# Performance work log

Measured on AMD Instinct MI355X. Metric: run time of the kernel, lower is better.

## Reference

```python
import jax, jax.numpy as jnp
import numpy as np

B, S, D = 64, 1024, 1024
NUM_TAGS = 33            # real IOBES tags
N = NUM_TAGS + 1         # + BOS tag
BOS = N - 1
NEG_INF = -10000.0


def setup_inputs() -> dict:
    key = jax.random.key(0)
    k1, k2, k3, k4 = jax.random.split(key, 4)
    emissions = jax.random.normal(k1, (B, S, D), dtype=jnp.float32)
    tags = jax.random.randint(k2, (B, S), 0, NUM_TAGS)          # valid real tags only
    mask = jnp.ones((B, S), dtype=jnp.float32)
    W = jax.random.normal(k3, (D, N), dtype=jnp.float32) / np.sqrt(D)
    b = jnp.zeros((N,), dtype=jnp.float32)
    transitions = jax.random.uniform(k4, (N, N), minval=-0.1, maxval=0.1, dtype=jnp.float32)
    # nothing may transition INTO the BOS tag
    transitions = transitions.at[:, BOS].set(NEG_INF)
    return {"emissions": emissions, "tags": tags, "mask": mask,
            "W": W, "b": b, "transitions": transitions}


def _crf_nll(em, tags, mask, transitions):
    """em: (B,S,N) projected emissions. Returns scalar NLL (sum over batch)."""
    # ---- gold path score ----
    first = tags[:, 0]                                          # (B,)
    score = transitions[BOS, first] + jnp.take_along_axis(em[:, 0], first[:, None], axis=1)[:, 0]
    e_t = jnp.take_along_axis(em[:, 1:], tags[:, 1:, None], axis=2)[..., 0]   # (B,S-1)
    t_t = transitions[tags[:, :-1], tags[:, 1:]]                 # (B,S-1)
    score = score + jnp.sum((e_t + t_t) * mask[:, 1:], axis=1)   # (B,)

    # ---- log partition via forward algorithm (scan over time) ----
    alphas0 = transitions[BOS][None, :] + em[:, 0]               # (B,N)

    def step(alphas, xs):
        em_t, m_t = xs                                           # (B,N), (B,)
        # scores[b, prev, nxt] = alphas[b,prev] + T[prev,nxt] + em_t[b,nxt]
        scores = alphas[:, :, None] + transitions[None] + em_t[:, None, :]
        new = jax.scipy.special.logsumexp(scores, axis=1)        # (B,N)
        m = m_t[:, None]
        return m * new + (1.0 - m) * alphas, None

    xs = (jnp.swapaxes(em[:, 1:], 0, 1), jnp.swapaxes(mask[:, 1:], 0, 1))  # time-major
    alphas, _ = jax.lax.scan(step, alphas0, xs)
    partition = jax.scipy.special.logsumexp(alphas, axis=1)      # (B,)
    return -jnp.sum(score - partition)


def reference(emissions, tags, mask, W, b, transitions):
    proj = emissions @ W + b                                     # (B,S,N), dropout p=0 is identity
    loss = _crf_nll(proj, tags, mask, transitions)
    logits = proj[:, :, :-1]                                     # drop BOS column, as in torch forward
    return loss, logits
```

## Files before the change

### kernel.cpp

```cpp
#include <hip/hip_runtime.h>
#include <math.h>

#define SS 1024
#define DD 1024
#define NB 64
#define NT 34
#define NP 48
#define NC 16
#define BOSR 33

typedef __attribute__((ext_vector_type(8))) short bf16x8;
typedef __attribute__((ext_vector_type(4))) float f32x4;

#define WS_BOS   0
#define WS_PMAT  (WS_BOS + NB*SS)
#define WS_CC    (WS_PMAT + NB*NC*NP*NP)
#define WS_Z     (WS_CC + NB*NC)
#define WS_SC    (WS_Z + NB)
#define WS_BF16  (WS_SC + NB)
#define BW_WT    0
#define BW_ETA   (48*1024)

__device__ __forceinline__ float warp_sum64(float x) {
  #pragma unroll
  for (int off = 32; off > 0; off >>= 1) x += __shfl_down(x, off, 64);
  return x;
}
__device__ __forceinline__ float rfl(float x) {
  return __int_as_float(__builtin_amdgcn_readfirstlane(__float_as_int(x)));
}
__device__ __forceinline__ unsigned short f2bf(float f) {
  unsigned int u = __float_as_uint(f);
  unsigned int r = u + 0x7fffu + ((u >> 16) & 1u);
  return (unsigned short)(r >> 16);
}
__device__ __forceinline__ float bf2f(unsigned short h) {
  return __uint_as_float(((unsigned int)h) << 16);
}

__global__ __launch_bounds__(256) void prep(const float* __restrict__ W,
                                            const float* __restrict__ T,
                                            unsigned short* __restrict__ bw) {
  int idx = blockIdx.x * 256 + threadIdx.x;
  if (idx < 48 * 1024) {
    int n = idx >> 10, k = idx & 1023;
    float v = (n < NT) ? W[k * NT + n] : 0.0f;
    bw[BW_WT + idx] = f2bf(v);
  } else if (idx < 48 * 1024 + 48 * 64) {
    int j = idx - 48 * 1024;
    int m = j >> 6, k = j & 63;
    float v = (m < NT && k < NT) ? __expf(T[k * NT + m]) : 0.0f;
    bw[BW_ETA + j] = f2bf(v);
  }
}

__global__ __launch_bounds__(256) void gemm_mfma(
    const float* __restrict__ em, const unsigned short* __restrict__ bw,
    const float* __restrict__ bias,
    float* __restrict__ logits, float* __restrict__ bos) {
  __shared__ unsigned short At[2][128][40];
  const int tid = threadIdx.x;
  const int lane = tid & 63, wv = tid >> 6;
  const int q = lane >> 4, l15 = lane & 15;
  const size_t row0 = (size_t)blockIdx.x * 128;
  const unsigned short* Wt = bw + BW_WT;
  const float4* g4 = (const float4*)(em + row0 * DD);

  f32x4 acc[2][3];
  f32x4 z4 = {0.f, 0.f, 0.f, 0.f};
  #pragma unroll
  for (int mt = 0; mt < 2; ++mt)
    #pragma unroll
    for (int nt = 0; nt < 3; ++nt) acc[mt][nt] = z4;

  int sr[4], sq[4];
  #pragma unroll
  for (int i = 0; i < 4; ++i) { int s = tid + i * 256; sr[i] = s >> 3; sq[i] = s & 7; }

  float4 pf[4];
  #pragma unroll
  for (int i = 0; i < 4; ++i) pf[i] = g4[sr[i] * 256 + sq[i]];
  bf16x8 Bf[3], Bn[3];
  #pragma unroll
  for (int nt = 0; nt < 3; ++nt)
    Bf[nt] = *(const bf16x8*)(Wt + (nt * 16 + l15) * 1024 + q * 8);

  for (int c = 0; c < 32; ++c) {
    #pragma unroll
    for (int i = 0; i < 4; ++i) {
      uint2 pk;
      pk.x = f2bf(pf[i].x) | ((unsigned int)f2bf(pf[i].y) << 16);
      pk.y = f2bf(pf[i].z) | ((unsigned int)f2bf(pf[i].w) << 16);
      *(uint2*)&At[c & 1][sr[i]][sq[i] * 4] = pk;
    }
    int cn = (c + 1 < 32) ? c + 1 : c;
    #pragma unroll
    for (int i = 0; i < 4; ++i) pf[i] = g4[sr[i] * 256 + cn * 8 + sq[i]];
    #pragma unroll
    for (int nt = 0; nt < 3; ++nt)
      Bn[nt] = *(const bf16x8*)(Wt + (nt * 16 + l15) * 1024 + cn * 32 + q * 8);
    __syncthreads();
    bf16x8 Af[2];
    #pragma unroll
    for (int mt = 0; mt < 2; ++mt)
      Af[mt] = *(const bf16x8*)&At[c & 1][wv * 32 + mt * 16 + l15][q * 8];
    #pragma unroll
    for (int mt = 0; mt < 2; ++mt)
      #pragma unroll
      for (int nt = 0; nt < 3; ++nt)
        acc[mt][nt] = __builtin_amdgcn_mfma_f32_16x16x32_bf16(
            Af[mt], Bf[nt], acc[mt][nt], 0, 0, 0);
    #pragma unroll
    for (int nt = 0; nt < 3; ++nt) Bf[nt] = Bn[nt];
  }

  #pragma unroll
  for (int nt = 0; nt < 3; ++nt) {
    int col = nt * 16 + l15;
    float bj = (col < NT) ? bias[col] : 0.0f;
    #pragma unroll
    for (int mt = 0; mt < 2; ++mt) {
      #pragma unroll
      for (int r = 0; r < 4; ++r) {
        float v = acc[mt][nt][r] + bj;
        size_t rg = row0 + wv * 32 + mt * 16 + q * 4 + r;
        if (col < 33) logits[rg * 33 + col] = v;
        else if (col == 33) bos[rg] = v;
      }
    }
  }
}

__global__ __launch_bounds__(64) void chains_mat(
    const float* __restrict__ logits, const float* __restrict__ bos,
    const unsigned short* __restrict__ bw, const float* __restrict__ mask,
    const float* __restrict__ T, const int* __restrict__ tags,
    float* __restrict__ Pmat, float* __restrict__ CC,
    float* __restrict__ scorearr) {
  const int blk = blockIdx.x, lane = threadIdx.x;
  if (blk >= NB * NC) {
    int b = blk - NB * NC;
    float local = 0.0f;
    for (int t = lane; t < SS; t += 64) {
      if (t == 0) {
        int tg = tags[b * SS];
        local += T[BOSR * NT + tg] + logits[(size_t)(b * SS) * 33 + tg];
      } else {
        int tg = tags[b * SS + t];
        int tp = tags[b * SS + t - 1];
        float m = mask[b * SS + t];
        local += m * (logits[(size_t)(b * SS + t) * 33 + tg] + T[tp * NT + tg]);
      }
    }
    float w = warp_sum64(local);
    if (lane == 0) scorearr[b] = w;
    return;
  }

  __shared__ unsigned short S[48][72];
  __shared__ float eeL[64][52];
  __shared__ float mk[64];
  const int b = blk >> 4, c = blk & 15;
  const int q = lane >> 4, l15 = lane & 15;

  {
    unsigned long long* p = (unsigned long long*)&S[0][0];
    for (int i = lane; i < 864; i += 64) p[i] = 0ull;
  }
  __syncthreads();
  if (lane < NT) S[lane][lane] = 0x3F80;

  int t = c * 64 + 1 + lane;
  if (t < SS) {
    size_t rg = (size_t)b * SS + t;
    #pragma unroll
    for (int j = 0; j < 33; ++j) eeL[lane][j] = __expf(logits[rg * 33 + j]);
    eeL[lane][33] = __expf(bos[rg]);
    #pragma unroll
    for (int j = 34; j < 48; ++j) eeL[lane][j] = 0.0f;
    mk[lane] = mask[rg];
  } else {
    #pragma unroll
    for (int j = 0; j < 48; ++j) eeL[lane][j] = 0.0f;
    mk[lane] = 0.0f;
  }

  bf16x8 Af[3][2];
  const unsigned short* eta = bw + BW_ETA;
  #pragma unroll
  for (int mt = 0; mt < 3; ++mt)
    #pragma unroll
    for (int kt = 0; kt < 2; ++kt)
      Af[mt][kt] = *(const bf16x8*)(eta + (mt * 16 + l15) * 64 + kt * 32 + q * 8);

  float Clog = 0.0f;
  __syncthreads();

  for (int tt = 0; tt < 64; ++tt) {
    float mval = mk[tt];
    if (mval > 0.5f) {
      bf16x8 Bf[2][3];
      #pragma unroll
      for (int kt = 0; kt < 2; ++kt)
        #pragma unroll
        for (int nt = 0; nt < 3; ++nt)
          Bf[kt][nt] = *(const bf16x8*)&S[nt * 16 + l15][kt * 32 + q * 8];
      f32x4 acc[3][3];
      f32x4 z4 = {0.f, 0.f, 0.f, 0.f};
      #pragma unroll
      for (int mt = 0; mt < 3; ++mt)
        #pragma unroll
        for (int nt = 0; nt < 3; ++nt) {
          acc[mt][nt] = __builtin_amdgcn_mfma_f32_16x16x32_bf16(
              Af[mt][0], Bf[0][nt], z4, 0, 0, 0);
          acc[mt][nt] = __builtin_amdgcn_mfma_f32_16x16x32_bf16(
              Af[mt][1], Bf[1][nt], acc[mt][nt], 0, 0, 0);
        }
      float r = rfl(acc[0][0][0]);
      float rin = __builtin_amdgcn_rcpf(r);
      float Cadd = __logf(r);
      #pragma unroll
      for (int mt = 0; mt < 3; ++mt) {
        f32x4 e4 = *(const f32x4*)&eeL[tt][mt * 16 + q * 4];
        e4 = e4 * rin;
        #pragma unroll
        for (int nt = 0; nt < 3; ++nt) {
          f32x4 v = acc[mt][nt] * e4;
          unsigned long long pk =
              (unsigned long long)f2bf(v[0]) |
              ((unsigned long long)f2bf(v[1]) << 16) |
              ((unsigned long long)f2bf(v[2]) << 32) |
              ((unsigned long long)f2bf(v[3]) << 48);
          *(unsigned long long*)&S[nt * 16 + l15][mt * 16 + q * 4] = pk;
        }
      }
      Clog += Cadd;
      __syncthreads();
    }
  }

  __syncthreads();
  float* Pb = Pmat + (size_t)(b * NC + c) * (NP * NP);
  #pragma unroll
  for (int i = 0; i < 9; ++i) {
    int flat = i * 64 + lane;
    int n = flat / 12, qq = flat - n * 12;
    unsigned long long pk = *(unsigned long long*)&S[n][qq * 4];
    float4 o;
    o.x = bf2f((unsigned short)(pk));
    o.y = bf2f((unsigned short)(pk >> 16));
    o.z = bf2f((unsigned short)(pk >> 32));
    o.w = bf2f((unsigned short)(pk >> 48));
    *(float4*)&Pb[n * 48 + qq * 4] = o;
  }
  if (lane == 0) CC[b * NC + c] = Clog;
}

__global__ __launch_bounds__(64) void reduceZ(
    const float* __restrict__ logits, const float* __restrict__ bos,
    const float* __restrict__ T, const float* __restrict__ Pmat,
    const float* __restrict__ CC, float* __restrict__ Zarr) {
  __shared__ float shv[64];
  const int b = blockIdx.x, lane = threadIdx.x;
  float a0;
  if (lane < 33)       a0 = logits[(size_t)b * SS * 33 + lane] + T[BOSR * NT + lane];
  else if (lane == 33) a0 = bos[(size_t)b * SS] + T[BOSR * NT + 33];
  else                 a0 = -INFINITY;
  float K = rfl(a0);
  float v = (lane < 48) ? __expf(a0 - K) : 0.0f;
  float C = K;
  for (int c = 0; c < NC; ++c) {
    shv[lane] = v;
    __syncthreads();
    float u = 0.0f;
    if (lane < 48) {
      const float* Pr = Pmat + (size_t)(b * NC + c) * (NP * NP) + lane * 48;
      #pragma unroll
      for (int qq = 0; qq < 12; ++qq) {
        float4 p4 = *(const float4*)(Pr + qq * 4);
        float4 v4 = *(const float4*)&shv[qq * 4];
        u = fmaf(p4.x, v4.x, u);
        u = fmaf(p4.y, v4.y, u);
        u = fmaf(p4.z, v4.z, u);
        u = fmaf(p4.w, v4.w, u);
      }
    }
    float r = rfl(u);
    v = u * __builtin_amdgcn_rcpf(r);
    C += __logf(r) + CC[b * NC + c];
    __syncthreads();
  }
  float s = warp_sum64(v);
  if (lane == 0) Zarr[b] = C + __logf(s);
}

__global__ void finalk(const float* __restrict__ Zarr,
                       const float* __restrict__ sc, float* __restrict__ out) {
  float x = Zarr[threadIdx.x] - sc[threadIdx.x];
  float s = warp_sum64(x);
  if (threadIdx.x == 0) out[0] = s;
}

extern "C" void kernel_launch(void* const* d_in, const int* in_sizes, int n_in,
                              void* d_out, int out_size, void* d_ws, size_t ws_size,
                              hipStream_t stream) {
  const float* em   = (const float*)d_in[0];
  const int*   tags = (const int*)d_in[1];
  const float* mask = (const float*)d_in[2];
  const float* W    = (const float*)d_in[3];
  const float* bias = (const float*)d_in[4];
  const float* T    = (const float*)d_in[5];

  float* out = (float*)d_out;
  float* ws  = (float*)d_ws;
  float* bos   = ws + WS_BOS;
  float* Pmat  = ws + WS_PMAT;
  float* CC    = ws + WS_CC;
  float* Zarr  = ws + WS_Z;
  float* score = ws + WS_SC;
  unsigned short* bw = (unsigned short*)(ws + WS_BF16);
  float* logits = out + 1;

  hipLaunchKernelGGL(prep, dim3(204), dim3(256), 0, stream, W, T, bw);
  hipLaunchKernelGGL(gemm_mfma, dim3(NB * SS / 128), dim3(256), 0, stream,
                     em, bw, bias, logits, bos);
  hipLaunchKernelGGL(chains_mat, dim3(NB * NC + NB), dim3(64), 0, stream,
                     logits, bos, bw, mask, T, tags, Pmat, CC, score);
  hipLaunchKernelGGL(reduceZ, dim3(NB), dim3(64), 0, stream,
                     logits, bos, T, Pmat, CC, Zarr);
  hipLaunchKernelGGL(finalk, dim3(1), dim3(64), 0, stream, Zarr, score, out);
}
```

Before: 460.2 us.

## Split CRF scan into more chunks, use packed bf16 converts and nontemporal loads

Doubles the number of time chunks per sequence (16 to 32) so the chunked forward-algorithm kernel runs 2048 blocks with 32 sequential MFMA steps each instead of 64, which shortens the serial critical path. It also replaces the mask shared-memory array with a wave ballot bitmask and swaps manual bf16 rounding for the hardware v_cvt_pk_bf16_f32 instruction. The emission loads in the GEMM become nontemporal, and the combine kernel's dot product is split across four accumulators. In exchange, the sequential combine kernel now has twice as many 48x48 matrix-vector steps, and twice as much Pmat is written and read.

```diff
diff --git a/kernel.cpp b/kernel.cpp
--- a/kernel.cpp
+++ b/kernel.cpp
@@ -6,7 +6,7 @@
 #define NB 64
 #define NT 34
 #define NP 48
-#define NC 16
+#define NC 32
 #define BOSR 33
 
 typedef __attribute__((ext_vector_type(8))) short bf16x8;
@@ -36,6 +36,11 @@
 }
 __device__ __forceinline__ float bf2f(unsigned short h) {
   return __uint_as_float(((unsigned int)h) << 16);
+}
+__device__ __forceinline__ unsigned int pk_bf16(float a, float b) {
+  unsigned int d;
+  asm("v_cvt_pk_bf16_f32 %0, %1, %2" : "=v"(d) : "v"(a), "v"(b));
+  return d;
 }
 
 __global__ __launch_bounds__(256) void prep(const float* __restrict__ W,
@@ -64,7 +69,7 @@
   const int q = lane >> 4, l15 = lane & 15;
   const size_t row0 = (size_t)blockIdx.x * 128;
   const unsigned short* Wt = bw + BW_WT;
-  const float4* g4 = (const float4*)(em + row0 * DD);
+  const f32x4* g4 = (const f32x4*)(em + row0 * DD);
 
   f32x4 acc[2][3];
   f32x4 z4 = {0.f, 0.f, 0.f, 0.f};
@@ -77,9 +82,10 @@
   #pragma unroll
   for (int i = 0; i < 4; ++i) { int s = tid + i * 256; sr[i] = s >> 3; sq[i] = s & 7; }
 
-  float4 pf[4];
-  #pragma unroll
-  for (int i = 0; i < 4; ++i) pf[i] = g4[sr[i] * 256 + sq[i]];
+  f32x4 pf[4];
+  #pragma unroll
+  for (int i = 0; i < 4; ++i)
+    pf[i] = __builtin_nontemporal_load(g4 + sr[i] * 256 + sq[i]);
   bf16x8 Bf[3], Bn[3];
   #pragma unroll
   for (int nt = 0; nt < 3; ++nt)
@@ -89,13 +95,14 @@
     #pragma unroll
     for (int i = 0; i < 4; ++i) {
       uint2 pk;
-      pk.x = f2bf(pf[i].x) | ((unsigned int)f2bf(pf[i].y) << 16);
-      pk.y = f2bf(pf[i].z) | ((unsigned int)f2bf(pf[i].w) << 16);
+      pk.x = pk_bf16(pf[i][0], pf[i][1]);
+      pk.y = pk_bf16(pf[i][2], pf[i][3]);
       *(uint2*)&At[c & 1][sr[i]][sq[i] * 4] = pk;
     }
     int cn = (c + 1 < 32) ? c + 1 : c;
     #pragma unroll
-    for (int i = 0; i < 4; ++i) pf[i] = g4[sr[i] * 256 + cn * 8 + sq[i]];
+    for (int i = 0; i < 4; ++i)
+      pf[i] = __builtin_nontemporal_load(g4 + sr[i] * 256 + cn * 8 + sq[i]);
     #pragma unroll
     for (int nt = 0; nt < 3; ++nt)
       Bn[nt] = *(const bf16x8*)(Wt + (nt * 16 + l15) * 1024 + cn * 32 + q * 8);
@@ -158,9 +165,8 @@
   }
 
   __shared__ unsigned short S[48][72];
-  __shared__ float eeL[64][52];
-  __shared__ float mk[64];
-  const int b = blk >> 4, c = blk & 15;
+  __shared__ float eeL[32][52];
+  const int b = blk >> 5, c = blk & 31;
   const int q = lane >> 4, l15 = lane & 15;
 
   {
@@ -170,20 +176,23 @@
   __syncthreads();
   if (lane < NT) S[lane][lane] = 0x3F80;
 
-  int t = c * 64 + 1 + lane;
-  if (t < SS) {
-    size_t rg = (size_t)b * SS + t;
-    #pragma unroll
-    for (int j = 0; j < 33; ++j) eeL[lane][j] = __expf(logits[rg * 33 + j]);
-    eeL[lane][33] = __expf(bos[rg]);
-    #pragma unroll
-    for (int j = 34; j < 48; ++j) eeL[lane][j] = 0.0f;
-    mk[lane] = mask[rg];
-  } else {
-    #pragma unroll
-    for (int j = 0; j < 48; ++j) eeL[lane][j] = 0.0f;
-    mk[lane] = 0.0f;
-  }
+  int t = c * 32 + 1 + lane;
+  float mval = 0.0f;
+  if (lane < 32) {
+    if (t < SS) {
+      size_t rg = (size_t)b * SS + t;
+      #pragma unroll
+      for (int j = 0; j < 33; ++j) eeL[lane][j] = __expf(logits[rg * 33 + j]);
+      eeL[lane][33] = __expf(bos[rg]);
+      #pragma unroll
+      for (int j = 34; j < 48; ++j) eeL[lane][j] = 0.0f;
+      mval = mask[rg];
+    } else {
+      #pragma unroll
+      for (int j = 0; j < 48; ++j) eeL[lane][j] = 0.0f;
+    }
+  }
+  unsigned long long mb = __ballot(mval > 0.5f);
 
   bf16x8 Af[3][2];
   const unsigned short* eta = bw + BW_ETA;
@@ -196,9 +205,8 @@
   float Clog = 0.0f;
   __syncthreads();
 
-  for (int tt = 0; tt < 64; ++tt) {
-    float mval = mk[tt];
-    if (mval > 0.5f) {
+  for (int tt = 0; tt < 32; ++tt) {
+    if ((mb >> tt) & 1ull) {
       bf16x8 Bf[2][3];
       #pragma unroll
       for (int kt = 0; kt < 2; ++kt)
@@ -226,12 +234,10 @@
         #pragma unroll
         for (int nt = 0; nt < 3; ++nt) {
           f32x4 v = acc[mt][nt] * e4;
-          unsigned long long pk =
-              (unsigned long long)f2bf(v[0]) |
-              ((unsigned long long)f2bf(v[1]) << 16) |
-              ((unsigned long long)f2bf(v[2]) << 32) |
-              ((unsigned long long)f2bf(v[3]) << 48);
-          *(unsigned long long*)&S[nt * 16 + l15][mt * 16 + q * 4] = pk;
+          uint2 pk;
+          pk.x = pk_bf16(v[0], v[1]);
+          pk.y = pk_bf16(v[2], v[3]);
+          *(uint2*)&S[nt * 16 + l15][mt * 16 + q * 4] = pk;
         }
       }
       Clog += Cadd;
@@ -275,15 +281,27 @@
     float u = 0.0f;
     if (lane < 48) {
       const float* Pr = Pmat + (size_t)(b * NC + c) * (NP * NP) + lane * 48;
-      #pragma unroll
-      for (int qq = 0; qq < 12; ++qq) {
-        float4 p4 = *(const float4*)(Pr + qq * 4);
-        float4 v4 = *(const float4*)&shv[qq * 4];
-        u = fmaf(p4.x, v4.x, u);
-        u = fmaf(p4.y, v4.y, u);
-        u = fmaf(p4.z, v4.z, u);
-        u = fmaf(p4.w, v4.w, u);
+      float uu0 = 0.f, uu1 = 0.f, uu2 = 0.f, uu3 = 0.f;
+      #pragma unroll
+      for (int qq = 0; qq < 12; qq += 4) {
+        float4 p0 = *(const float4*)(Pr + qq * 4);
+        float4 p1 = *(const float4*)(Pr + qq * 4 + 4);
+        float4 p2 = *(const float4*)(Pr + qq * 4 + 8);
+        float4 p3 = *(const float4*)(Pr + qq * 4 + 12);
+        float4 v0 = *(const float4*)&shv[qq * 4];
+        float4 v1 = *(const float4*)&shv[qq * 4 + 4];
+        float4 v2 = *(const float4*)&shv[qq * 4 + 8];
+        float4 v3 = *(const float4*)&shv[qq * 4 + 12];
+        uu0 = fmaf(p0.x, v0.x, uu0); uu0 = fmaf(p0.y, v0.y, uu0);
+        uu0 = fmaf(p0.z, v0.z, uu0); uu0 = fmaf(p0.w, v0.w, uu0);
+        uu1 = fmaf(p1.x, v1.x, uu1); uu1 = fmaf(p1.y, v1.y, uu1);
+        uu1 = fmaf(p1.z, v1.z, uu1); uu1 = fmaf(p1.w, v1.w, uu1);
+        uu2 = fmaf(p2.x, v2.x, uu2); uu2 = fmaf(p2.y, v2.y, uu2);
+        uu2 = fmaf(p2.z, v2.z, uu2); uu2 = fmaf(p2.w, v2.w, uu2);
+        uu3 = fmaf(p3.x, v3.x, uu3); uu3 = fmaf(p3.y, v3.y, uu3);
+        uu3 = fmaf(p3.w, v3.w, uu3); uu3 = fmaf(p3.z, v3.z, uu3);
       }
+      u = (uu0 + uu1) + (uu2 + uu3);
     }
     float r = rfl(u);
     v = u * __builtin_amdgcn_rcpf(r);
```

Measured after the change: 417.8 us. 9.2% less time.
